# Kernel tuning notes

Measured on AMD Instinct MI355X. Metric: run time of the kernel, lower is better.

The kernel has to match this reference:

```python
import jax, jax.numpy as jnp
import numpy as np

TAU_B = 0.5
MARGIN_M = 0.5
ETA = 1.0
LAM_IN = 1.0
LAM_OV = 1.0
LAM_DIV = 0.5


def setup_inputs() -> dict:
    key = jax.random.key(0)
    k1, k2, k3 = jax.random.split(key, 3)
    N, D, C, K = 131072, 256, 100, 2
    z = jax.random.normal(k1, (N, D), dtype=jnp.float32)
    labels = jax.random.randint(k2, (N,), 0, C, dtype=jnp.int64)
    ball_centers = jax.random.normal(k3, (C, K, D), dtype=jnp.float32) * 0.1
    ball_radii = jnp.ones((C, K), dtype=jnp.float32) * 0.5
    return {"z": z, "labels": labels, "ball_centers": ball_centers, "ball_radii": ball_radii}


def reference(z, labels, ball_centers, ball_radii):
    radii = jnp.abs(ball_radii) + 1e-6  # [C, K]

    # ---- intra term: softmax-weighted squared distance to own-class balls ----
    c = ball_centers[labels]            # [N, K, D]
    r = radii[labels]                   # [N, K]
    dist_sq = jnp.sum((z[:, None, :] - c) ** 2, axis=-1)   # [N, K]
    q = jax.nn.softmax(-dist_sq / TAU_B, axis=-1)           # [N, K]
    dist_sq_w = jnp.sum(q * dist_sq, axis=-1)               # [N]
    r_sq_w = jnp.sum(q * r ** 2, axis=-1)                   # [N]
    L_intra = jnp.mean(jax.nn.relu(dist_sq_w - ETA * r_sq_w))

    # ---- overlap term: all ordered pairs of distinct balls ----
    C_, K_, D = ball_centers.shape
    M = C_ * K_
    cf = ball_centers.reshape(M, D)
    rf = radii.reshape(M)
    dsq = jnp.sum((cf[:, None, :] - cf[None, :, :]) ** 2, axis=-1)  # [M, M]
    eye = jnp.eye(M, dtype=bool)
    d = jnp.sqrt(jnp.where(eye, 1.0, dsq))  # safe sqrt on diagonal
    ov = jax.nn.relu(rf[:, None] + rf[None, :] + MARGIN_M - d)
    L_overlap = jnp.sum(jnp.where(eye, 0.0, ov)) / max(M * (M - 1), 1)

    # ---- diversity term: within-class ball pairs p < q ----
    dsq_c = jnp.sum((ball_centers[:, :, None, :] - ball_centers[:, None, :, :]) ** 2, axis=-1)  # [C, K, K]
    triu = jnp.triu(jnp.ones((K_, K_), dtype=bool), 1)
    dc = jnp.sqrt(jnp.where(triu, dsq_c, 1.0))
    L_div = jnp.sum(jnp.where(triu, jax.nn.relu(1.0 - dc), 0.0)) / max(C_ * K_ * (K_ - 1) // 2, 1)

    total = LAM_IN * L_intra + LAM_OV * L_overlap + LAM_DIV * L_div
    return jnp.stack([total, L_intra, L_overlap, L_div])
```

## Files before the change

### kernel.cpp

```cpp
#include <hip/hip_runtime.h>
#include <math.h>

#define N_SAMPLES 131072
#define DIM 256
#define C_CLASSES 100
#define K_BALLS 2
#define M_BALLS 200
#define TAU_B 0.5f
#define MARGIN_M 0.5f

#define SLOT_STRIDE 16
#define WS_INTRA 0
#define WS_OV 128
#define WS_DV 256
#define WS_TOTAL 384

__global__ void zero_ws_kernel(double* ws) {
    const int t = blockIdx.x * blockDim.x + threadIdx.x;
    if (t < WS_TOTAL) ws[t] = 0.0;
}

__device__ __forceinline__ void acc_sq(const float4 x, const float4 y, float& d) {
    float t;
    t = x.x - y.x; d = fmaf(t, t, d);
    t = x.y - y.y; d = fmaf(t, t, d);
    t = x.z - y.z; d = fmaf(t, t, d);
    t = x.w - y.w; d = fmaf(t, t, d);
}

__global__ __launch_bounds__(256, 4) void intra_kernel(
    const float* __restrict__ z,
    const int* __restrict__ labels,
    const float* __restrict__ centers,
    const float* __restrict__ radii_raw,
    double* __restrict__ ws)
{
    __shared__ float wsum[4];
    const int lane = threadIdx.x & 63;
    const int wv = threadIdx.x >> 6;
    const int gwave = (blockIdx.x * blockDim.x + threadIdx.x) >> 6;
    const int grp = lane >> 4;
    const int sl = lane & 15;
    const int base = gwave * 16;

    const int lab = labels[base + sl];

    float acc = 0.0f;

    for (int it = 0; it < 4; ++it) {
        const int n = base + it * 4 + grp;
        const int lbl = __shfl(lab, it * 4 + grp, 64);

        const float* zp = z + (size_t)n * DIM + sl * 4;
        const float* cp = centers + (size_t)lbl * (2 * DIM) + sl * 4;

        const float4 z0 = *(const float4*)(zp);
        const float4 z1 = *(const float4*)(zp + 64);
        const float4 z2 = *(const float4*)(zp + 128);
        const float4 z3 = *(const float4*)(zp + 192);
        const float4 a0 = *(const float4*)(cp);
        const float4 a1 = *(const float4*)(cp + 64);
        const float4 a2 = *(const float4*)(cp + 128);
        const float4 a3 = *(const float4*)(cp + 192);
        const float4 b0 = *(const float4*)(cp + 256);
        const float4 b1 = *(const float4*)(cp + 320);
        const float4 b2 = *(const float4*)(cp + 384);
        const float4 b3 = *(const float4*)(cp + 448);

        float d0 = 0.0f, d1 = 0.0f;
        acc_sq(z0, a0, d0); acc_sq(z1, a1, d0); acc_sq(z2, a2, d0); acc_sq(z3, a3, d0);
        acc_sq(z0, b0, d1); acc_sq(z1, b1, d1); acc_sq(z2, b2, d1); acc_sq(z3, b3, d1);

        #pragma unroll
        for (int m = 1; m <= 8; m <<= 1) {
            d0 += __shfl_xor(d0, m, 64);
            d1 += __shfl_xor(d1, m, 64);
        }

        if (sl == 0) {
            const float r0 = fabsf(radii_raw[lbl * 2 + 0]) + 1e-6f;
            const float r1 = fabsf(radii_raw[lbl * 2 + 1]) + 1e-6f;
            const float s0 = -d0 * 2.0f;
            const float s1 = -d1 * 2.0f;
            const float mx = fmaxf(s0, s1);
            const float e0 = expf(s0 - mx);
            const float e1 = expf(s1 - mx);
            const float inv = 1.0f / (e0 + e1);
            const float q0 = e0 * inv, q1 = e1 * inv;
            const float dsw = q0 * d0 + q1 * d1;
            const float rsw = q0 * r0 * r0 + q1 * r1 * r1;
            acc += fmaxf(dsw - rsw, 0.0f);
        }
    }

    acc += __shfl_xor(acc, 16, 64);
    acc += __shfl_xor(acc, 32, 64);
    if (lane == 0) wsum[wv] = acc;
    __syncthreads();
    if (threadIdx.x == 0) {
        const float s = wsum[0] + wsum[1] + wsum[2] + wsum[3];
        atomicAdd(&ws[WS_INTRA + (blockIdx.x & 7) * SLOT_STRIDE], (double)s);
    }
}

__global__ __launch_bounds__(256) void pair_kernel(
    const float* __restrict__ centers,
    const float* __restrict__ radii_raw,
    double* __restrict__ ws)
{
    __shared__ float s_ov[4], s_dv[4];
    const int lane = threadIdx.x & 63;
    const int wv = threadIdx.x >> 6;
    const int grp = lane >> 4;
    const int sl = lane & 15;
    const int i = blockIdx.x;
    const int j = blockIdx.y * 16 + wv * 4 + grp;
    const int jc = j < M_BALLS ? j : M_BALLS - 1;

    const float* ip = centers + (size_t)i * DIM + sl * 4;
    const float* jp = centers + (size_t)jc * DIM + sl * 4;

    const float4 i0 = *(const float4*)(ip);
    const float4 i1 = *(const float4*)(ip + 64);
    const float4 i2 = *(const float4*)(ip + 128);
    const float4 i3 = *(const float4*)(ip + 192);
    const float4 j0 = *(const float4*)(jp);
    const float4 j1 = *(const float4*)(jp + 64);
    const float4 j2 = *(const float4*)(jp + 128);
    const float4 j3 = *(const float4*)(jp + 192);

    float s = 0.0f;
    acc_sq(i0, j0, s); acc_sq(i1, j1, s); acc_sq(i2, j2, s); acc_sq(i3, j3, s);

    #pragma unroll
    for (int m = 1; m <= 8; m <<= 1)
        s += __shfl_xor(s, m, 64);

    float ov = 0.0f, dv = 0.0f;
    if (sl == 0 && j < M_BALLS && j != i) {
        const float d = sqrtf(s);
        const float ri = fabsf(radii_raw[i]) + 1e-6f;
        const float rj = fabsf(radii_raw[j]) + 1e-6f;
        ov = fmaxf(ri + rj + MARGIN_M - d, 0.0f);
        if (((i & 1) == 0) && (j == i + 1))
            dv = fmaxf(1.0f - d, 0.0f);
    }
    ov += __shfl_xor(ov, 16, 64);
    ov += __shfl_xor(ov, 32, 64);
    dv += __shfl_xor(dv, 16, 64);
    dv += __shfl_xor(dv, 32, 64);

    if (lane == 0) { s_ov[wv] = ov; s_dv[wv] = dv; }
    __syncthreads();
    if (threadIdx.x == 0) {
        const float o = s_ov[0] + s_ov[1] + s_ov[2] + s_ov[3];
        const float d2 = s_dv[0] + s_dv[1] + s_dv[2] + s_dv[3];
        const int slot = (blockIdx.x & 7) * SLOT_STRIDE;
        if (o != 0.0f) atomicAdd(&ws[WS_OV + slot], (double)o);
        if (d2 != 0.0f) atomicAdd(&ws[WS_DV + slot], (double)d2);
    }
}

__global__ void finalize_kernel(const double* __restrict__ ws, float* __restrict__ out) {
    double si = 0.0, so = 0.0, sd = 0.0;
    for (int s = 0; s < 8; ++s) {
        si += ws[WS_INTRA + s * SLOT_STRIDE];
        so += ws[WS_OV + s * SLOT_STRIDE];
        sd += ws[WS_DV + s * SLOT_STRIDE];
    }
    const double L_intra = si / (double)N_SAMPLES;
    const double L_overlap = so / (double)(M_BALLS * (M_BALLS - 1));
    const double L_div = sd / (double)(C_CLASSES * K_BALLS * (K_BALLS - 1) / 2);
    const double total = L_intra + L_overlap + 0.5 * L_div;
    out[0] = (float)total;
    out[1] = (float)L_intra;
    out[2] = (float)L_overlap;
    out[3] = (float)L_div;
}

extern "C" void kernel_launch(void* const* d_in, const int* in_sizes, int n_in,
                              void* d_out, int out_size, void* d_ws, size_t ws_size,
                              hipStream_t stream) {
    const float* z = (const float*)d_in[0];
    const int* labels = (const int*)d_in[1];
    const float* centers = (const float*)d_in[2];
    const float* radii = (const float*)d_in[3];
    float* out = (float*)d_out;
    double* ws = (double*)d_ws;

    zero_ws_kernel<<<2, 256, 0, stream>>>(ws);
    intra_kernel<<<2048, 256, 0, stream>>>(z, labels, centers, radii, ws);
    pair_kernel<<<dim3(200, 13), 256, 0, stream>>>(centers, radii, ws);
    finalize_kernel<<<1, 1, 0, stream>>>(ws, out);
}
```

Before: 203.0 us.

## Merge intra and pair kernels into one launch with per-block partials

Combines the intra-class and pairwise-ball kernels into a single grid whose blocks branch on index, and drops the workspace-zeroing kernel. Each block now writes its partial sum to its own workspace slot instead of doing double atomics, and the finalize kernel becomes a 256-thread parallel reduction over those slots. This cuts the launch count from four to two and removes atomic contention, at the cost of a larger finalize reduction and the removal of the occupancy hint on the intra path.

```diff
diff --git a/kernel.cpp b/kernel.cpp
--- a/kernel.cpp
+++ b/kernel.cpp
@@ -6,19 +6,14 @@
 #define C_CLASSES 100
 #define K_BALLS 2
 #define M_BALLS 200
-#define TAU_B 0.5f
 #define MARGIN_M 0.5f
 
-#define SLOT_STRIDE 16
-#define WS_INTRA 0
-#define WS_OV 128
-#define WS_DV 256
-#define WS_TOTAL 384
+#define NB_INTRA 2048
+#define JCHUNKS 13
+#define NB_PAIR (M_BALLS * JCHUNKS)
 
-__global__ void zero_ws_kernel(double* ws) {
-    const int t = blockIdx.x * blockDim.x + threadIdx.x;
-    if (t < WS_TOTAL) ws[t] = 0.0;
-}
+#define WS_OV_OFF 2048
+#define WS_DV_OFF (2048 + NB_PAIR)
 
 __device__ __forceinline__ void acc_sq(const float4 x, const float4 y, float& d) {
     float t;
@@ -28,154 +23,164 @@
     t = x.w - y.w; d = fmaf(t, t, d);
 }
 
-__global__ __launch_bounds__(256, 4) void intra_kernel(
+__global__ __launch_bounds__(256) void main_kernel(
     const float* __restrict__ z,
     const int* __restrict__ labels,
     const float* __restrict__ centers,
     const float* __restrict__ radii_raw,
     double* __restrict__ ws)
 {
-    __shared__ float wsum[4];
-    const int lane = threadIdx.x & 63;
-    const int wv = threadIdx.x >> 6;
-    const int gwave = (blockIdx.x * blockDim.x + threadIdx.x) >> 6;
-    const int grp = lane >> 4;
-    const int sl = lane & 15;
-    const int base = gwave * 16;
-
-    const int lab = labels[base + sl];
-
-    float acc = 0.0f;
-
-    for (int it = 0; it < 4; ++it) {
-        const int n = base + it * 4 + grp;
-        const int lbl = __shfl(lab, it * 4 + grp, 64);
-
-        const float* zp = z + (size_t)n * DIM + sl * 4;
-        const float* cp = centers + (size_t)lbl * (2 * DIM) + sl * 4;
-
-        const float4 z0 = *(const float4*)(zp);
-        const float4 z1 = *(const float4*)(zp + 64);
-        const float4 z2 = *(const float4*)(zp + 128);
-        const float4 z3 = *(const float4*)(zp + 192);
-        const float4 a0 = *(const float4*)(cp);
-        const float4 a1 = *(const float4*)(cp + 64);
-        const float4 a2 = *(const float4*)(cp + 128);
-        const float4 a3 = *(const float4*)(cp + 192);
-        const float4 b0 = *(const float4*)(cp + 256);
-        const float4 b1 = *(const float4*)(cp + 320);
-        const float4 b2 = *(const float4*)(cp + 384);
-        const float4 b3 = *(const float4*)(cp + 448);
-
-        float d0 = 0.0f, d1 = 0.0f;
-        acc_sq(z0, a0, d0); acc_sq(z1, a1, d0); acc_sq(z2, a2, d0); acc_sq(z3, a3, d0);
-        acc_sq(z0, b0, d1); acc_sq(z1, b1, d1); acc_sq(z2, b2, d1); acc_sq(z3, b3, d1);
-
-        #pragma unroll
-        for (int m = 1; m <= 8; m <<= 1) {
-            d0 += __shfl_xor(d0, m, 64);
-            d1 += __shfl_xor(d1, m, 64);
-        }
-
-        if (sl == 0) {
-            const float r0 = fabsf(radii_raw[lbl * 2 + 0]) + 1e-6f;
-            const float r1 = fabsf(radii_raw[lbl * 2 + 1]) + 1e-6f;
-            const float s0 = -d0 * 2.0f;
-            const float s1 = -d1 * 2.0f;
-            const float mx = fmaxf(s0, s1);
-            const float e0 = expf(s0 - mx);
-            const float e1 = expf(s1 - mx);
-            const float inv = 1.0f / (e0 + e1);
-            const float q0 = e0 * inv, q1 = e1 * inv;
-            const float dsw = q0 * d0 + q1 * d1;
-            const float rsw = q0 * r0 * r0 + q1 * r1 * r1;
-            acc += fmaxf(dsw - rsw, 0.0f);
-        }
-    }
-
-    acc += __shfl_xor(acc, 16, 64);
-    acc += __shfl_xor(acc, 32, 64);
-    if (lane == 0) wsum[wv] = acc;
-    __syncthreads();
-    if (threadIdx.x == 0) {
-        const float s = wsum[0] + wsum[1] + wsum[2] + wsum[3];
-        atomicAdd(&ws[WS_INTRA + (blockIdx.x & 7) * SLOT_STRIDE], (double)s);
-    }
-}
-
-__global__ __launch_bounds__(256) void pair_kernel(
-    const float* __restrict__ centers,
-    const float* __restrict__ radii_raw,
-    double* __restrict__ ws)
-{
-    __shared__ float s_ov[4], s_dv[4];
+    __shared__ float sh[8];
     const int lane = threadIdx.x & 63;
     const int wv = threadIdx.x >> 6;
     const int grp = lane >> 4;
     const int sl = lane & 15;
-    const int i = blockIdx.x;
-    const int j = blockIdx.y * 16 + wv * 4 + grp;
-    const int jc = j < M_BALLS ? j : M_BALLS - 1;
 
-    const float* ip = centers + (size_t)i * DIM + sl * 4;
-    const float* jp = centers + (size_t)jc * DIM + sl * 4;
+    if (blockIdx.x < NB_INTRA) {
+        const int gwave = blockIdx.x * 4 + wv;
+        const int base = gwave * 16;
 
-    const float4 i0 = *(const float4*)(ip);
-    const float4 i1 = *(const float4*)(ip + 64);
-    const float4 i2 = *(const float4*)(ip + 128);
-    const float4 i3 = *(const float4*)(ip + 192);
-    const float4 j0 = *(const float4*)(jp);
-    const float4 j1 = *(const float4*)(jp + 64);
-    const float4 j2 = *(const float4*)(jp + 128);
-    const float4 j3 = *(const float4*)(jp + 192);
+        const int lab = labels[base + sl];
 
-    float s = 0.0f;
-    acc_sq(i0, j0, s); acc_sq(i1, j1, s); acc_sq(i2, j2, s); acc_sq(i3, j3, s);
+        float acc = 0.0f;
 
-    #pragma unroll
-    for (int m = 1; m <= 8; m <<= 1)
-        s += __shfl_xor(s, m, 64);
+        #pragma unroll
+        for (int it = 0; it < 4; ++it) {
+            const int n = base + it * 4 + grp;
+            const int lbl = __shfl(lab, it * 4 + grp, 64);
 
-    float ov = 0.0f, dv = 0.0f;
-    if (sl == 0 && j < M_BALLS && j != i) {
-        const float d = sqrtf(s);
-        const float ri = fabsf(radii_raw[i]) + 1e-6f;
-        const float rj = fabsf(radii_raw[j]) + 1e-6f;
-        ov = fmaxf(ri + rj + MARGIN_M - d, 0.0f);
-        if (((i & 1) == 0) && (j == i + 1))
-            dv = fmaxf(1.0f - d, 0.0f);
-    }
-    ov += __shfl_xor(ov, 16, 64);
-    ov += __shfl_xor(ov, 32, 64);
-    dv += __shfl_xor(dv, 16, 64);
-    dv += __shfl_xor(dv, 32, 64);
+            const float* zp = z + (size_t)n * DIM + sl * 4;
+            const float* cp = centers + (size_t)lbl * (2 * DIM) + sl * 4;
 
-    if (lane == 0) { s_ov[wv] = ov; s_dv[wv] = dv; }
-    __syncthreads();
-    if (threadIdx.x == 0) {
-        const float o = s_ov[0] + s_ov[1] + s_ov[2] + s_ov[3];
-        const float d2 = s_dv[0] + s_dv[1] + s_dv[2] + s_dv[3];
-        const int slot = (blockIdx.x & 7) * SLOT_STRIDE;
-        if (o != 0.0f) atomicAdd(&ws[WS_OV + slot], (double)o);
-        if (d2 != 0.0f) atomicAdd(&ws[WS_DV + slot], (double)d2);
+            const float4 z0 = *(const float4*)(zp);
+            const float4 z1 = *(const float4*)(zp + 64);
+            const float4 z2 = *(const float4*)(zp + 128);
+            const float4 z3 = *(const float4*)(zp + 192);
+            const float4 a0 = *(const float4*)(cp);
+            const float4 a1 = *(const float4*)(cp + 64);
+            const float4 a2 = *(const float4*)(cp + 128);
+            const float4 a3 = *(const float4*)(cp + 192);
+            const float4 b0 = *(const float4*)(cp + 256);
+            const float4 b1 = *(const float4*)(cp + 320);
+            const float4 b2 = *(const float4*)(cp + 384);
+            const float4 b3 = *(const float4*)(cp + 448);
+
+            float d0 = 0.0f, d1 = 0.0f;
+            acc_sq(z0, a0, d0); acc_sq(z1, a1, d0); acc_sq(z2, a2, d0); acc_sq(z3, a3, d0);
+            acc_sq(z0, b0, d1); acc_sq(z1, b1, d1); acc_sq(z2, b2, d1); acc_sq(z3, b3, d1);
+
+            #pragma unroll
+            for (int m = 1; m <= 8; m <<= 1) {
+                d0 += __shfl_xor(d0, m, 64);
+                d1 += __shfl_xor(d1, m, 64);
+            }
+
+            if (sl == 0) {
+                const float r0 = fabsf(radii_raw[lbl * 2 + 0]) + 1e-6f;
+                const float r1 = fabsf(radii_raw[lbl * 2 + 1]) + 1e-6f;
+                const float s0 = -d0 * 2.0f;
+                const float s1 = -d1 * 2.0f;
+                const float mx = fmaxf(s0, s1);
+                const float e0 = expf(s0 - mx);
+                const float e1 = expf(s1 - mx);
+                const float inv = 1.0f / (e0 + e1);
+                const float q0 = e0 * inv, q1 = e1 * inv;
+                const float dsw = q0 * d0 + q1 * d1;
+                const float rsw = q0 * r0 * r0 + q1 * r1 * r1;
+                acc += fmaxf(dsw - rsw, 0.0f);
+            }
+        }
+
+        acc += __shfl_xor(acc, 16, 64);
+        acc += __shfl_xor(acc, 32, 64);
+        if (lane == 0) sh[wv] = acc;
+        __syncthreads();
+        if (threadIdx.x == 0)
+            ws[blockIdx.x] = (double)(sh[0] + sh[1] + sh[2] + sh[3]);
+    } else {
+        const int pb = blockIdx.x - NB_INTRA;
+        const int i = pb / JCHUNKS;
+        const int jchunk = pb - i * JCHUNKS;
+        const int j = jchunk * 16 + wv * 4 + grp;
+        const int jc = j < M_BALLS ? j : M_BALLS - 1;
+
+        const float* ip = centers + (size_t)i * DIM + sl * 4;
+        const float* jp = centers + (size_t)jc * DIM + sl * 4;
+
+        const float4 i0 = *(const float4*)(ip);
+        const float4 i1 = *(const float4*)(ip + 64);
+        const float4 i2 = *(const float4*)(ip + 128);
+        const float4 i3 = *(const float4*)(ip + 192);
+        const float4 j0 = *(const float4*)(jp);
+        const float4 j1 = *(const float4*)(jp + 64);
+        const float4 j2 = *(const float4*)(jp + 128);
+        const float4 j3 = *(const float4*)(jp + 192);
+
+        float s = 0.0f;
+        acc_sq(i0, j0, s); acc_sq(i1, j1, s); acc_sq(i2, j2, s); acc_sq(i3, j3, s);
+
+        #pragma unroll
+        for (int m = 1; m <= 8; m <<= 1)
+            s += __shfl_xor(s, m, 64);
+
+        float ov = 0.0f, dv = 0.0f;
+        if (sl == 0 && j < M_BALLS && j != i) {
+            const float d = sqrtf(s);
+            const float ri = fabsf(radii_raw[i]) + 1e-6f;
+            const float rj = fabsf(radii_raw[j]) + 1e-6f;
+            ov = fmaxf(ri + rj + MARGIN_M - d, 0.0f);
+            if (((i & 1) == 0) && (j == i + 1))
+                dv = fmaxf(1.0f - d, 0.0f);
+        }
+        ov += __shfl_xor(ov, 16, 64);
+        ov += __shfl_xor(ov, 32, 64);
+        dv += __shfl_xor(dv, 16, 64);
+        dv += __shfl_xor(dv, 32, 64);
+
+        if (lane == 0) { sh[wv] = ov; sh[4 + wv] = dv; }
+        __syncthreads();
+        if (threadIdx.x == 0) {
+            ws[WS_OV_OFF + pb] = (double)(sh[0] + sh[1] + sh[2] + sh[3]);
+            ws[WS_DV_OFF + pb] = (double)(sh[4] + sh[5] + sh[6] + sh[7]);
+        }
     }
 }
 
-__global__ void finalize_kernel(const double* __restrict__ ws, float* __restrict__ out) {
+__global__ __launch_bounds__(256) void finalize_kernel(
+    const double* __restrict__ ws, float* __restrict__ out)
+{
+    __shared__ double shi[4], sho[4], shd[4];
+    const int t = threadIdx.x;
+    const int lane = t & 63;
+    const int wv = t >> 6;
+
     double si = 0.0, so = 0.0, sd = 0.0;
-    for (int s = 0; s < 8; ++s) {
-        si += ws[WS_INTRA + s * SLOT_STRIDE];
-        so += ws[WS_OV + s * SLOT_STRIDE];
-        sd += ws[WS_DV + s * SLOT_STRIDE];
+    for (int k = t; k < NB_INTRA; k += 256) si += ws[k];
+    for (int k = t; k < NB_PAIR; k += 256) {
+        so += ws[WS_OV_OFF + k];
+        sd += ws[WS_DV_OFF + k];
     }
-    const double L_intra = si / (double)N_SAMPLES;
-    const double L_overlap = so / (double)(M_BALLS * (M_BALLS - 1));
-    const double L_div = sd / (double)(C_CLASSES * K_BALLS * (K_BALLS - 1) / 2);
-    const double total = L_intra + L_overlap + 0.5 * L_div;
-    out[0] = (float)total;
-    out[1] = (float)L_intra;
-    out[2] = (float)L_overlap;
-    out[3] = (float)L_div;
+    #pragma unroll
+    for (int m = 1; m <= 32; m <<= 1) {
+        si += __shfl_xor(si, m, 64);
+        so += __shfl_xor(so, m, 64);
+        sd += __shfl_xor(sd, m, 64);
+    }
+    if (lane == 0) { shi[wv] = si; sho[wv] = so; shd[wv] = sd; }
+    __syncthreads();
+    if (t == 0) {
+        const double ti = shi[0] + shi[1] + shi[2] + shi[3];
+        const double to = sho[0] + sho[1] + sho[2] + sho[3];
+        const double td = shd[0] + shd[1] + shd[2] + shd[3];
+        const double L_intra = ti / (double)N_SAMPLES;
+        const double L_overlap = to / (double)(M_BALLS * (M_BALLS - 1));
+        const double L_div = td / (double)(C_CLASSES * K_BALLS * (K_BALLS - 1) / 2);
+        const double total = L_intra + L_overlap + 0.5 * L_div;
+        out[0] = (float)total;
+        out[1] = (float)L_intra;
+        out[2] = (float)L_overlap;
+        out[3] = (float)L_div;
+    }
 }
 
 extern "C" void kernel_launch(void* const* d_in, const int* in_sizes, int n_in,
@@ -188,8 +193,6 @@
     float* out = (float*)d_out;
     double* ws = (double*)d_ws;
 
-    zero_ws_kernel<<<2, 256, 0, stream>>>(ws);
-    intra_kernel<<<2048, 256, 0, stream>>>(z, labels, centers, radii, ws);
-    pair_kernel<<<dim3(200, 13), 256, 0, stream>>>(centers, radii, ws);
-    finalize_kernel<<<1, 1, 0, stream>>>(ws, out);
+    main_kernel<<<NB_INTRA + NB_PAIR, 256, 0, stream>>>(z, labels, centers, radii, ws);
+    finalize_kernel<<<1, 256, 0, stream>>>(ws, out);
 }
```

Measured after the change: 204.8 us. Within noise of the previous version (+0.9%).
